# Kernel optimization log

Hardware: AMD Instinct MI355X
Metric: run time of the kernel (lower is better)

## Reference

```python
import jax, jax.numpy as jnp
import numpy as np

B, S, H, W, L = 16, 2048, 512, 4, 2  # batch, seq, projection_dim, width, n_layers
EPS = 1e-5


def _ln(x, g, b):
    m = jnp.mean(x, axis=-1, keepdims=True)
    v = jnp.mean((x - m) ** 2, axis=-1, keepdims=True)
    return g * (x - m) * jax.lax.rsqrt(v + EPS) + b


def setup_inputs() -> dict:
    key = jax.random.key(0)
    ks = jax.random.split(key, 24)
    s = 0.02
    d = {
        'inputs': jax.random.normal(ks[0], (B, S, H), jnp.float32),
        'left_padding': jax.random.normal(ks[1], (W, H), jnp.float32) * s,
        'right_padding': jax.random.normal(ks[2], (W, H), jnp.float32) * s,
        'Wl': jax.random.normal(ks[3], (W * H, H), jnp.float32) * s,
        'bl': jnp.zeros((H,), jnp.float32),
        'Wr': jax.random.normal(ks[4], (W * H, H), jnp.float32) * s,
        'br': jnp.zeros((H,), jnp.float32),
        'lw1': jax.random.normal(ks[5], (L, H, H), jnp.float32) * s,
        'lb1': jnp.zeros((L, H), jnp.float32),
        'lw2': jax.random.normal(ks[6], (L, H, H), jnp.float32) * s,
        'lb2': jnp.zeros((L, H), jnp.float32),
        'lg': jnp.ones((L, H), jnp.float32),
        'lbeta': jnp.zeros((L, H), jnp.float32),
        'rw1': jax.random.normal(ks[7], (L, H, H), jnp.float32) * s,
        'rb1': jnp.zeros((L, H), jnp.float32),
        'rw2': jax.random.normal(ks[8], (L, H, H), jnp.float32) * s,
        'rb2': jnp.zeros((L, H), jnp.float32),
        'rg': jnp.ones((L, H), jnp.float32),
        'rbeta': jnp.zeros((L, H), jnp.float32),
    }
    return d


def reference(inputs, left_padding, right_padding, Wl, bl, Wr, br,
              lw1, lb1, lw2, lb2, lg, lbeta,
              rw1, rb1, rw2, rb2, rg, rbeta):
    b, s, h = inputs.shape
    w = left_padding.shape[0]
    padded = jnp.concatenate([
        jnp.broadcast_to(left_padding, (b, w, h)), inputs,
        jnp.broadcast_to(right_padding, (b, w, h))], axis=1)  # [B, W+S+W, H]
    t = jnp.arange(s)[:, None]
    off = jnp.arange(w)[None, :]
    left = padded[:, t + off].reshape(b, s, w * h)           # rows [t, t+w)
    right = padded[:, t + (w + 1) + off].reshape(b, s, w * h)  # rows [t+w+1, t+2w+1)
    lo = jax.nn.relu(jnp.einsum('bsk,kh->bsh', left, Wl) + bl)
    ro = jax.nn.relu(jnp.einsum('bsk,kh->bsh', right, Wr) + br)
    layers = []
    for i in range(lw1.shape[0]):
        # SublayerConnection: x + FF(LayerNorm(x)); FF = w2(relu(w1(.)))
        lo = lo + jnp.einsum('bsh,hk->bsk', jax.nn.relu(
            jnp.einsum('bsh,hk->bsk', _ln(lo, lg[i], lbeta[i]), lw1[i]) + lb1[i]), lw2[i]) + lb2[i]
        ro = ro + jnp.einsum('bsh,hk->bsk', jax.nn.relu(
            jnp.einsum('bsh,hk->bsk', _ln(ro, rg[i], rbeta[i]), rw1[i]) + rb1[i]), rw2[i]) + rb2[i]
        layers.append(jnp.concatenate([lo, ro], axis=-1))  # [B,S,2H]
    stacked = jnp.stack(layers, axis=0)                 # [L,B,S,2H]
    all_layers = jnp.transpose(stacked, (0, 2, 1, 3))   # [L,S,B,2H]
    last_layers = layers[-1]                            # [B,S,2H]
    return all_layers, last_layers
```

## Files before the change

kernel.cpp:

```cpp
#include <hip/hip_runtime.h>
#include <stdint.h>

#define Bx   16
#define Sx   2048
#define Hx   512
#define Lx   2
#define PHx  2056
#define Mx   32768

typedef float f32x4  __attribute__((ext_vector_type(4)));
typedef __bf16 bf16x8 __attribute__((ext_vector_type(8)));
typedef unsigned short u16x8 __attribute__((ext_vector_type(8)));

typedef __attribute__((address_space(1))) void gvoid_t;
typedef __attribute__((address_space(3))) void lvoid_t;

__device__ __forceinline__ unsigned short f2bf(float f) {
  uint32_t u = __float_as_uint(f);
  u += 0x7FFFu + ((u >> 16) & 1u);
  return (unsigned short)(u >> 16);
}

__global__ __launch_bounds__(256) void build_padded_k(
    const float* __restrict__ inp, const float* __restrict__ lp,
    const float* __restrict__ rp, unsigned short* __restrict__ padded) {
  int64_t idx = (int64_t)blockIdx.x * 256 + threadIdx.x;
  int h = (int)(idx & 511);
  int64_t rowi = idx >> 9;
  int r = (int)(rowi % 2056);
  int b = (int)(rowi / 2056);
  float v;
  if (r < 4)          v = lp[r * 512 + h];
  else if (r < 2052)  v = inp[((int64_t)b * 2048 + (r - 4)) * 512 + h];
  else                v = rp[(r - 2052) * 512 + h];
  padded[idx] = f2bf(v);
}

__global__ __launch_bounds__(256) void prep_weights_k(
    const float* __restrict__ Wl, const float* __restrict__ Wr,
    const float* __restrict__ lw1, const float* __restrict__ lw2,
    const float* __restrict__ rw1, const float* __restrict__ rw2,
    unsigned short* __restrict__ Wlt, unsigned short* __restrict__ Wrt,
    unsigned short* __restrict__ lw1t, unsigned short* __restrict__ lw2t,
    unsigned short* __restrict__ rw1t, unsigned short* __restrict__ rw2t) {
  int idx = blockIdx.x * 256 + threadIdx.x;
  if (idx < 2097152) {
    int j = idx & 1048575;
    const float* src = (idx < 1048576) ? Wl : Wr;
    unsigned short* dst = (idx < 1048576) ? Wlt : Wrt;
    int n = j >> 11, k = j & 2047;
    dst[j] = f2bf(src[(int64_t)k * 512 + n]);
  } else {
    int j = idx - 2097152;
    int mat = j >> 18;
    int e = j & 262143;
    int arr = mat >> 1, layer = mat & 1;
    const float* srcs[4] = {lw1, lw2, rw1, rw2};
    unsigned short* dsts[4] = {lw1t, lw2t, rw1t, rw2t};
    const float* src = srcs[arr] + (int64_t)layer * 262144;
    unsigned short* dst = dsts[arr] + (int64_t)layer * 262144;
    int n = e >> 9, k = e & 511;
    dst[e] = f2bf(src[k * 512 + n]);
  }
}

__global__ __launch_bounds__(256) void ln_k(
    const float* __restrict__ x, int x_off,
    const float* __restrict__ g, const float* __restrict__ beta,
    unsigned short* __restrict__ xhat) {
  int row = blockIdx.x * 4 + (threadIdx.x >> 6);
  int lane = threadIdx.x & 63;
  const float4* xr = (const float4*)(x + (int64_t)row * 1024 + x_off);
  float4 u = xr[lane * 2], w = xr[lane * 2 + 1];
  float xs[8] = {u.x, u.y, u.z, u.w, w.x, w.y, w.z, w.w};
  float sum = 0.f, ss = 0.f;
#pragma unroll
  for (int t = 0; t < 8; t++) { sum += xs[t]; ss += xs[t] * xs[t]; }
#pragma unroll
  for (int o = 32; o > 0; o >>= 1) {
    sum += __shfl_xor(sum, o);
    ss  += __shfl_xor(ss, o);
  }
  float mean = sum * (1.0f / 512.0f);
  float var  = ss * (1.0f / 512.0f) - mean * mean;
  float rstd = rsqrtf(var + 1e-5f);
  const float4* g4 = (const float4*)g;
  const float4* b4 = (const float4*)beta;
  float4 ga = g4[lane * 2], gb = g4[lane * 2 + 1];
  float4 ba = b4[lane * 2], bb = b4[lane * 2 + 1];
  float gs[8] = {ga.x, ga.y, ga.z, ga.w, gb.x, gb.y, gb.z, gb.w};
  float bs[8] = {ba.x, ba.y, ba.z, ba.w, bb.x, bb.y, bb.z, bb.w};
  u16x8 val;
#pragma unroll
  for (int t = 0; t < 8; t++) val[t] = f2bf(gs[t] * (xs[t] - mean) * rstd + bs[t]);
  *(u16x8*)(xhat + (int64_t)row * 512 + lane * 8) = val;
}

template <int MODE>
__global__ __launch_bounds__(256) void gemm_k(
    const unsigned short* __restrict__ A, int64_t a_bstride, int a_off, int K,
    const unsigned short* __restrict__ Bt, const float* __restrict__ bias,
    float* __restrict__ C, unsigned short* __restrict__ Cb,
    int c_off, float* __restrict__ out0p) {
  __shared__ unsigned short sA[128 * 32];
  __shared__ unsigned short sB[128 * 32];
  const int tid  = threadIdx.x;
  const int lane = tid & 63;
  const int wave = tid >> 6;
  const int m0 = blockIdx.x * 128;
  const int n0 = blockIdx.y * 128;
  const int wm = (wave >> 1) * 64;
  const int wn = (wave & 1) * 64;
  const int fr = lane >> 4;
  const int fc = lane & 15;

  const unsigned short* Ablk =
      A + (int64_t)(m0 >> 11) * a_bstride + (int64_t)(m0 & 2047) * 512 + a_off;
  const unsigned short* Bblk = Bt + (int64_t)n0 * K;

  f32x4 acc[4][4] = {};

  const int t0 = tid, t1 = tid + 256;
  const int ar0 = t0 >> 2, ac0 = (t0 & 3) * 8;
  const int ar1 = t1 >> 2, ac1 = (t1 & 3) * 8;

  for (int k0 = 0; k0 < K; k0 += 32) {
    __builtin_amdgcn_global_load_lds(
        (gvoid_t*)(Ablk + (int64_t)ar0 * 512 + k0 + ac0),
        (lvoid_t*)(sA + t0 * 8), 16, 0, 0);
    __builtin_amdgcn_global_load_lds(
        (gvoid_t*)(Ablk + (int64_t)ar1 * 512 + k0 + ac1),
        (lvoid_t*)(sA + t1 * 8), 16, 0, 0);
    __builtin_amdgcn_global_load_lds(
        (gvoid_t*)(Bblk + (int64_t)ar0 * K + k0 + ac0),
        (lvoid_t*)(sB + t0 * 8), 16, 0, 0);
    __builtin_amdgcn_global_load_lds(
        (gvoid_t*)(Bblk + (int64_t)ar1 * K + k0 + ac1),
        (lvoid_t*)(sB + t1 * 8), 16, 0, 0);
    __syncthreads();

    bf16x8 af[4], bf[4];
#pragma unroll
    for (int i = 0; i < 4; i++)
      af[i] = *(const bf16x8*)(sA + (wm + i * 16 + fc) * 32 + fr * 8);
#pragma unroll
    for (int j = 0; j < 4; j++)
      bf[j] = *(const bf16x8*)(sB + (wn + j * 16 + fc) * 32 + fr * 8);
#pragma unroll
    for (int i = 0; i < 4; i++)
#pragma unroll
      for (int j = 0; j < 4; j++)
        acc[i][j] = __builtin_amdgcn_mfma_f32_16x16x32_bf16(af[i], bf[j], acc[i][j], 0, 0, 0);
    __syncthreads();
  }

  int col[4];
  float bv[4];
#pragma unroll
  for (int j = 0; j < 4; j++) {
    col[j] = n0 + wn + j * 16 + fc;
    bv[j] = bias[col[j]];
  }
  const int b_idx = m0 >> 11;
#pragma unroll
  for (int i = 0; i < 4; i++) {
#pragma unroll
    for (int r = 0; r < 4; r++) {
      const int m = m0 + wm + i * 16 + fr * 4 + r;
      if (MODE == 0) {
        const int64_t base = (int64_t)m * 1024 + c_off;
#pragma unroll
        for (int j = 0; j < 4; j++) {
          float v = acc[i][j][r] + bv[j];
          C[base + col[j]] = v > 0.f ? v : 0.f;
        }
      } else if (MODE == 1) {
        const int64_t base = (int64_t)m * 512;
#pragma unroll
        for (int j = 0; j < 4; j++) {
          float v = acc[i][j][r] + bv[j];
          Cb[base + col[j]] = f2bf(v > 0.f ? v : 0.f);
        }
      } else {
        const int64_t base = (int64_t)m * 1024 + c_off;
        const int s = m & 2047;
        const int64_t obase = (int64_t)s * 16384 + (int64_t)b_idx * 1024 + c_off;
#pragma unroll
        for (int j = 0; j < 4; j++) {
          float v = C[base + col[j]] + acc[i][j][r] + bv[j];
          C[base + col[j]] = v;
          out0p[obase + col[j]] = v;
        }
      }
    }
  }
}

extern "C" void kernel_launch(void* const* d_in, const int* in_sizes, int n_in,
                              void* d_out, int out_size, void* d_ws, size_t ws_size,
                              hipStream_t stream) {
  const float* inputs = (const float*)d_in[0];
  const float* lp     = (const float*)d_in[1];
  const float* rp     = (const float*)d_in[2];
  const float* Wl     = (const float*)d_in[3];
  const float* bl     = (const float*)d_in[4];
  const float* Wr     = (const float*)d_in[5];
  const float* br     = (const float*)d_in[6];
  const float* lw1    = (const float*)d_in[7];
  const float* lb1    = (const float*)d_in[8];
  const float* lw2    = (const float*)d_in[9];
  const float* lb2    = (const float*)d_in[10];
  const float* lg     = (const float*)d_in[11];
  const float* lbeta  = (const float*)d_in[12];
  const float* rw1    = (const float*)d_in[13];
  const float* rb1    = (const float*)d_in[14];
  const float* rw2    = (const float*)d_in[15];
  const float* rb2    = (const float*)d_in[16];
  const float* rg     = (const float*)d_in[17];
  const float* rbeta  = (const float*)d_in[18];

  float* out0 = (float*)d_out;
  float* out1 = out0 + (int64_t)Lx * Sx * Bx * 1024;

  char* w = (char*)d_ws;
  auto take = [&](size_t n) { char* p = w; w += (n + 255) & ~(size_t)255; return p; };
  unsigned short* padded = (unsigned short*)take((size_t)Bx * PHx * Hx * 2);
  unsigned short* Wlt    = (unsigned short*)take(2048ull * 512 * 2);
  unsigned short* Wrt    = (unsigned short*)take(2048ull * 512 * 2);
  unsigned short* lw1t   = (unsigned short*)take((size_t)Lx * 512 * 512 * 2);
  unsigned short* lw2t   = (unsigned short*)take((size_t)Lx * 512 * 512 * 2);
  unsigned short* rw1t   = (unsigned short*)take((size_t)Lx * 512 * 512 * 2);
  unsigned short* rw2t   = (unsigned short*)take((size_t)Lx * 512 * 512 * 2);
  unsigned short* xhat   = (unsigned short*)take((size_t)Mx * 512 * 2);
  unsigned short* hidden = (unsigned short*)take((size_t)Mx * 512 * 2);

  build_padded_k<<<65792, 256, 0, stream>>>(inputs, lp, rp, padded);
  prep_weights_k<<<16384, 256, 0, stream>>>(Wl, Wr, lw1, lw2, rw1, rw2,
                                            Wlt, Wrt, lw1t, lw2t, rw1t, rw2t);

  dim3 gg(256, 4);
  gemm_k<0><<<gg, 256, 0, stream>>>(padded, (int64_t)PHx * 512, 0, 2048, Wlt, bl,
                                    out1, nullptr, 0, nullptr);
  gemm_k<0><<<gg, 256, 0, stream>>>(padded, (int64_t)PHx * 512, 5 * 512, 2048, Wrt, br,
                                    out1, nullptr, 512, nullptr);

  for (int i = 0; i < Lx; i++) {
    for (int side = 0; side < 2; side++) {
      const float* g  = (side ? rg : lg) + i * 512;
      const float* be = (side ? rbeta : lbeta) + i * 512;
      const float* b1 = (side ? rb1 : lb1) + i * 512;
      const float* b2 = (side ? rb2 : lb2) + i * 512;
      const unsigned short* w1t = (side ? rw1t : lw1t) + (int64_t)i * 262144;
      const unsigned short* w2t = (side ? rw2t : lw2t) + (int64_t)i * 262144;

      ln_k<<<8192, 256, 0, stream>>>(out1, side * 512, g, be, xhat);
      gemm_k<1><<<gg, 256, 0, stream>>>(xhat, (int64_t)2048 * 512, 0, 512, w1t, b1,
                                        nullptr, hidden, 0, nullptr);
      gemm_k<2><<<gg, 256, 0, stream>>>(hidden, (int64_t)2048 * 512, 0, 512, w2t, b2,
                                        out1, nullptr, side * 512,
                                        out0 + (int64_t)i * Sx * Bx * 1024);
    }
  }
}
```

Before: 1.183 ms.

## Fuse LayerNorm into FFN GEMM via epilogue row stats, batch left/right sides

Removes the standalone LayerNorm kernel. The producing GEMM epilogues now write per-row partial sum and sum-of-squares, and the first FFN GEMM normalizes fp32 state rows while staging A into LDS. Left and right branches are batched into a single launch via blockIdx.z, which halves the launch count and doubles the grid. The padding build is vectorized and the weight transpose goes through LDS tiles. The cost is extra fp32 reads inside the GEMM A-load path (no async LDS load for A) and a one-pass variance formula.

```diff
diff --git a/kernel.cpp b/kernel.cpp
--- a/kernel.cpp
+++ b/kernel.cpp
@@ -24,16 +24,21 @@
 __global__ __launch_bounds__(256) void build_padded_k(
     const float* __restrict__ inp, const float* __restrict__ lp,
     const float* __restrict__ rp, unsigned short* __restrict__ padded) {
-  int64_t idx = (int64_t)blockIdx.x * 256 + threadIdx.x;
+  int64_t idx = ((int64_t)blockIdx.x * 256 + threadIdx.x) * 8;
   int h = (int)(idx & 511);
   int64_t rowi = idx >> 9;
   int r = (int)(rowi % 2056);
   int b = (int)(rowi / 2056);
-  float v;
-  if (r < 4)          v = lp[r * 512 + h];
-  else if (r < 2052)  v = inp[((int64_t)b * 2048 + (r - 4)) * 512 + h];
-  else                v = rp[(r - 2052) * 512 + h];
-  padded[idx] = f2bf(v);
+  const float* src;
+  if (r < 4)          src = lp + r * 512 + h;
+  else if (r < 2052)  src = inp + ((int64_t)b * 2048 + (r - 4)) * 512 + h;
+  else                src = rp + (r - 2052) * 512 + h;
+  float4 u = ((const float4*)src)[0];
+  float4 w = ((const float4*)src)[1];
+  u16x8 o;
+  o[0] = f2bf(u.x); o[1] = f2bf(u.y); o[2] = f2bf(u.z); o[3] = f2bf(u.w);
+  o[4] = f2bf(w.x); o[5] = f2bf(w.y); o[6] = f2bf(w.z); o[7] = f2bf(w.w);
+  *(u16x8*)(padded + idx) = o;
 }
 
 __global__ __launch_bounds__(256) void prep_weights_k(
@@ -43,65 +48,168 @@
     unsigned short* __restrict__ Wlt, unsigned short* __restrict__ Wrt,
     unsigned short* __restrict__ lw1t, unsigned short* __restrict__ lw2t,
     unsigned short* __restrict__ rw1t, unsigned short* __restrict__ rw2t) {
-  int idx = blockIdx.x * 256 + threadIdx.x;
-  if (idx < 2097152) {
-    int j = idx & 1048575;
-    const float* src = (idx < 1048576) ? Wl : Wr;
-    unsigned short* dst = (idx < 1048576) ? Wlt : Wrt;
-    int n = j >> 11, k = j & 2047;
-    dst[j] = f2bf(src[(int64_t)k * 512 + n]);
+  __shared__ unsigned short tl[32][36];
+  int b = blockIdx.x;
+  const float* src; unsigned short* dst; int K, tk, tn;
+  if (b < 2048) {
+    src = (b < 1024) ? Wl : Wr;
+    dst = (b < 1024) ? Wlt : Wrt;
+    int t = b & 1023; tk = t >> 4; tn = t & 15; K = 2048;
   } else {
-    int j = idx - 2097152;
-    int mat = j >> 18;
-    int e = j & 262143;
-    int arr = mat >> 1, layer = mat & 1;
-    const float* srcs[4] = {lw1, lw2, rw1, rw2};
-    unsigned short* dsts[4] = {lw1t, lw2t, rw1t, rw2t};
-    const float* src = srcs[arr] + (int64_t)layer * 262144;
-    unsigned short* dst = dsts[arr] + (int64_t)layer * 262144;
-    int n = e >> 9, k = e & 511;
-    dst[e] = f2bf(src[k * 512 + n]);
-  }
-}
-
-__global__ __launch_bounds__(256) void ln_k(
-    const float* __restrict__ x, int x_off,
-    const float* __restrict__ g, const float* __restrict__ beta,
-    unsigned short* __restrict__ xhat) {
-  int row = blockIdx.x * 4 + (threadIdx.x >> 6);
-  int lane = threadIdx.x & 63;
-  const float4* xr = (const float4*)(x + (int64_t)row * 1024 + x_off);
-  float4 u = xr[lane * 2], w = xr[lane * 2 + 1];
-  float xs[8] = {u.x, u.y, u.z, u.w, w.x, w.y, w.z, w.w};
-  float sum = 0.f, ss = 0.f;
-#pragma unroll
-  for (int t = 0; t < 8; t++) { sum += xs[t]; ss += xs[t] * xs[t]; }
-#pragma unroll
-  for (int o = 32; o > 0; o >>= 1) {
-    sum += __shfl_xor(sum, o);
-    ss  += __shfl_xor(ss, o);
-  }
-  float mean = sum * (1.0f / 512.0f);
-  float var  = ss * (1.0f / 512.0f) - mean * mean;
-  float rstd = rsqrtf(var + 1e-5f);
-  const float4* g4 = (const float4*)g;
-  const float4* b4 = (const float4*)beta;
-  float4 ga = g4[lane * 2], gb = g4[lane * 2 + 1];
-  float4 ba = b4[lane * 2], bb = b4[lane * 2 + 1];
-  float gs[8] = {ga.x, ga.y, ga.z, ga.w, gb.x, gb.y, gb.z, gb.w};
-  float bs[8] = {ba.x, ba.y, ba.z, ba.w, bb.x, bb.y, bb.z, bb.w};
-  u16x8 val;
-#pragma unroll
-  for (int t = 0; t < 8; t++) val[t] = f2bf(gs[t] * (xs[t] - mean) * rstd + bs[t]);
-  *(u16x8*)(xhat + (int64_t)row * 512 + lane * 8) = val;
-}
-
-template <int MODE>
+    int b2 = b - 2048;
+    int mat = b2 >> 8;
+    const float* srcs[8] = {lw1, lw1 + 262144, lw2, lw2 + 262144,
+                            rw1, rw1 + 262144, rw2, rw2 + 262144};
+    unsigned short* dsts[8] = {lw1t, lw1t + 262144, lw2t, lw2t + 262144,
+                               rw1t, rw1t + 262144, rw2t, rw2t + 262144};
+    src = srcs[mat]; dst = dsts[mat];
+    int tt = b2 & 255; tk = tt >> 4; tn = tt & 15; K = 512;
+  }
+  int t = threadIdx.x;
+  int rr = t >> 3, c4 = (t & 7) * 4;
+  float4 v = *(const float4*)(src + (int64_t)(tk * 32 + rr) * 512 + tn * 32 + c4);
+  tl[c4 + 0][rr] = f2bf(v.x);
+  tl[c4 + 1][rr] = f2bf(v.y);
+  tl[c4 + 2][rr] = f2bf(v.z);
+  tl[c4 + 3][rr] = f2bf(v.w);
+  __syncthreads();
+  int nn = t >> 3, k4 = (t & 7) * 4;
+  ushort4 o = {tl[nn][k4], tl[nn][k4 + 1], tl[nn][k4 + 2], tl[nn][k4 + 3]};
+  *(ushort4*)(dst + (int64_t)(tn * 32 + nn) * K + tk * 32 + k4) = o;
+}
+
+template <int MODE, bool STATS>
 __global__ __launch_bounds__(256) void gemm_k(
-    const unsigned short* __restrict__ A, int64_t a_bstride, int a_off, int K,
-    const unsigned short* __restrict__ Bt, const float* __restrict__ bias,
-    float* __restrict__ C, unsigned short* __restrict__ Cb,
-    int c_off, float* __restrict__ out0p) {
+    const unsigned short* __restrict__ A0, const unsigned short* __restrict__ A1,
+    int64_t a_bstride, int a_off_per_z, int K,
+    const unsigned short* __restrict__ Bt0, const unsigned short* __restrict__ Bt1,
+    const float* __restrict__ bias0, const float* __restrict__ bias1,
+    float* __restrict__ C, float* __restrict__ out0p, float* __restrict__ P) {
+  __shared__ unsigned short sA[128 * 32];
+  __shared__ unsigned short sB[128 * 32];
+  __shared__ float sls[128][2][2];
+  const int tid  = threadIdx.x;
+  const int lane = tid & 63;
+  const int wave = tid >> 6;
+  const int m0 = blockIdx.x * 128;
+  const int n0 = blockIdx.y * 128;
+  const int z  = blockIdx.z;
+  const int wm = (wave >> 1) * 64;
+  const int wn = (wave & 1) * 64;
+  const int fr = lane >> 4;
+  const int fc = lane & 15;
+
+  const unsigned short* A  = z ? A1 : A0;
+  const unsigned short* Bt = z ? Bt1 : Bt0;
+  const float* bias = z ? bias1 : bias0;
+  const int a_off = z * a_off_per_z;
+  const int c_off = z * 512;
+
+  const unsigned short* Ablk =
+      A + (int64_t)(m0 >> 11) * a_bstride + (int64_t)(m0 & 2047) * 512 + a_off;
+  const unsigned short* Bblk = Bt + (int64_t)n0 * K;
+
+  f32x4 acc[4][4] = {};
+
+  const int t0 = tid, t1 = tid + 256;
+  const int ar0 = t0 >> 2, ac0 = (t0 & 3) * 8;
+  const int ar1 = t1 >> 2, ac1 = (t1 & 3) * 8;
+
+  for (int k0 = 0; k0 < K; k0 += 32) {
+    __builtin_amdgcn_global_load_lds(
+        (gvoid_t*)(Ablk + (int64_t)ar0 * 512 + k0 + ac0),
+        (lvoid_t*)(sA + t0 * 8), 16, 0, 0);
+    __builtin_amdgcn_global_load_lds(
+        (gvoid_t*)(Ablk + (int64_t)ar1 * 512 + k0 + ac1),
+        (lvoid_t*)(sA + t1 * 8), 16, 0, 0);
+    __builtin_amdgcn_global_load_lds(
+        (gvoid_t*)(Bblk + (int64_t)ar0 * K + k0 + ac0),
+        (lvoid_t*)(sB + t0 * 8), 16, 0, 0);
+    __builtin_amdgcn_global_load_lds(
+        (gvoid_t*)(Bblk + (int64_t)ar1 * K + k0 + ac1),
+        (lvoid_t*)(sB + t1 * 8), 16, 0, 0);
+    __syncthreads();
+
+    bf16x8 af[4], bf[4];
+#pragma unroll
+    for (int i = 0; i < 4; i++)
+      af[i] = *(const bf16x8*)(sA + (wm + i * 16 + fc) * 32 + fr * 8);
+#pragma unroll
+    for (int j = 0; j < 4; j++)
+      bf[j] = *(const bf16x8*)(sB + (wn + j * 16 + fc) * 32 + fr * 8);
+#pragma unroll
+    for (int i = 0; i < 4; i++)
+#pragma unroll
+      for (int j = 0; j < 4; j++)
+        acc[i][j] = __builtin_amdgcn_mfma_f32_16x16x32_bf16(af[i], bf[j], acc[i][j], 0, 0, 0);
+    __syncthreads();
+  }
+
+  int col[4];
+  float bv[4];
+#pragma unroll
+  for (int j = 0; j < 4; j++) {
+    col[j] = n0 + wn + j * 16 + fc;
+    bv[j] = bias[col[j]];
+  }
+  const int b_idx = m0 >> 11;
+#pragma unroll
+  for (int i = 0; i < 4; i++) {
+#pragma unroll
+    for (int r = 0; r < 4; r++) {
+      const int m = m0 + wm + i * 16 + fr * 4 + r;
+      const int64_t base = (int64_t)m * 1024 + c_off;
+      float vs[4];
+      if (MODE == 0) {
+#pragma unroll
+        for (int j = 0; j < 4; j++) {
+          float v = acc[i][j][r] + bv[j];
+          v = v > 0.f ? v : 0.f;
+          C[base + col[j]] = v;
+          vs[j] = v;
+        }
+      } else {
+        const int s = m & 2047;
+        const int64_t obase = (int64_t)s * 16384 + (int64_t)b_idx * 1024 + c_off;
+#pragma unroll
+        for (int j = 0; j < 4; j++) {
+          float v = C[base + col[j]] + acc[i][j][r] + bv[j];
+          C[base + col[j]] = v;
+          out0p[obase + col[j]] = v;
+          vs[j] = v;
+        }
+      }
+      if (STATS) {
+        float s1 = vs[0] + vs[1] + vs[2] + vs[3];
+        float s2 = vs[0] * vs[0] + vs[1] * vs[1] + vs[2] * vs[2] + vs[3] * vs[3];
+#pragma unroll
+        for (int o = 1; o < 16; o <<= 1) {
+          s1 += __shfl_xor(s1, o);
+          s2 += __shfl_xor(s2, o);
+        }
+        if (fc == 0) {
+          int li = (wave >> 1) * 64 + i * 16 + fr * 4 + r;
+          sls[li][wave & 1][0] = s1;
+          sls[li][wave & 1][1] = s2;
+        }
+      }
+    }
+  }
+  if (STATS) {
+    __syncthreads();
+    int li = tid >> 1, comp = tid & 1;
+    float v = sls[li][0][comp] + sls[li][1][comp];
+    P[(((int64_t)z * 4 + blockIdx.y) * Mx + m0 + li) * 2 + comp] = v;
+  }
+}
+
+__global__ __launch_bounds__(256) void gemm_ln_k(
+    const float* __restrict__ state, const float* __restrict__ P,
+    const float* __restrict__ g0, const float* __restrict__ g1p,
+    const float* __restrict__ be0, const float* __restrict__ be1,
+    const unsigned short* __restrict__ Bt0, const unsigned short* __restrict__ Bt1,
+    const float* __restrict__ bias0, const float* __restrict__ bias1,
+    unsigned short* __restrict__ hidden) {
   __shared__ unsigned short sA[128 * 32];
   __shared__ unsigned short sB[128 * 32];
   const int tid  = threadIdx.x;
@@ -109,34 +217,72 @@
   const int wave = tid >> 6;
   const int m0 = blockIdx.x * 128;
   const int n0 = blockIdx.y * 128;
+  const int z  = blockIdx.z;
   const int wm = (wave >> 1) * 64;
   const int wn = (wave & 1) * 64;
   const int fr = lane >> 4;
   const int fc = lane & 15;
 
-  const unsigned short* Ablk =
-      A + (int64_t)(m0 >> 11) * a_bstride + (int64_t)(m0 & 2047) * 512 + a_off;
-  const unsigned short* Bblk = Bt + (int64_t)n0 * K;
+  const unsigned short* Bt = z ? Bt1 : Bt0;
+  const float* bias = z ? bias1 : bias0;
+  const float* g    = z ? g1p : g0;
+  const float* be   = z ? be1 : be0;
+  const int c_off = z * 512;
+  const unsigned short* Bblk = Bt + (int64_t)n0 * 512;
+
+  const int row  = tid >> 1;
+  const int half = tid & 1;
+  const int m = m0 + row;
+  const float* srcrow = state + (int64_t)m * 1024 + c_off + half * 16;
+
+  float s1 = 0.f, s2 = 0.f;
+#pragma unroll
+  for (int nb = 0; nb < 4; nb++) {
+    s1 += P[(((int64_t)z * 4 + nb) * Mx + m) * 2 + 0];
+    s2 += P[(((int64_t)z * 4 + nb) * Mx + m) * 2 + 1];
+  }
+  const float mean = s1 * (1.0f / 512.0f);
+  const float rstd = rsqrtf(s2 * (1.0f / 512.0f) - mean * mean + 1e-5f);
 
   f32x4 acc[4][4] = {};
 
   const int t0 = tid, t1 = tid + 256;
-  const int ar0 = t0 >> 2, ac0 = (t0 & 3) * 8;
-  const int ar1 = t1 >> 2, ac1 = (t1 & 3) * 8;
-
-  for (int k0 = 0; k0 < K; k0 += 32) {
-    __builtin_amdgcn_global_load_lds(
-        (gvoid_t*)(Ablk + (int64_t)ar0 * 512 + k0 + ac0),
-        (lvoid_t*)(sA + t0 * 8), 16, 0, 0);
-    __builtin_amdgcn_global_load_lds(
-        (gvoid_t*)(Ablk + (int64_t)ar1 * 512 + k0 + ac1),
-        (lvoid_t*)(sA + t1 * 8), 16, 0, 0);
-    __builtin_amdgcn_global_load_lds(
-        (gvoid_t*)(Bblk + (int64_t)ar0 * K + k0 + ac0),
+  const int br0 = t0 >> 2, bc0 = (t0 & 3) * 8;
+  const int br1 = t1 >> 2, bc1 = (t1 & 3) * 8;
+
+  for (int k0 = 0; k0 < 512; k0 += 32) {
+    __builtin_amdgcn_global_load_lds(
+        (gvoid_t*)(Bblk + (int64_t)br0 * 512 + k0 + bc0),
         (lvoid_t*)(sB + t0 * 8), 16, 0, 0);
     __builtin_amdgcn_global_load_lds(
-        (gvoid_t*)(Bblk + (int64_t)ar1 * K + k0 + ac1),
+        (gvoid_t*)(Bblk + (int64_t)br1 * 512 + k0 + bc1),
         (lvoid_t*)(sB + t1 * 8), 16, 0, 0);
+
+    const float* sp = srcrow + k0;
+    float xs[16], gs[16], bs[16];
+    *(float4*)(xs + 0)  = ((const float4*)sp)[0];
+    *(float4*)(xs + 4)  = ((const float4*)sp)[1];
+    *(float4*)(xs + 8)  = ((const float4*)sp)[2];
+    *(float4*)(xs + 12) = ((const float4*)sp)[3];
+    const float* gp = g + k0 + half * 16;
+    const float* bp = be + k0 + half * 16;
+    *(float4*)(gs + 0)  = ((const float4*)gp)[0];
+    *(float4*)(gs + 4)  = ((const float4*)gp)[1];
+    *(float4*)(gs + 8)  = ((const float4*)gp)[2];
+    *(float4*)(gs + 12) = ((const float4*)gp)[3];
+    *(float4*)(bs + 0)  = ((const float4*)bp)[0];
+    *(float4*)(bs + 4)  = ((const float4*)bp)[1];
+    *(float4*)(bs + 8)  = ((const float4*)bp)[2];
+    *(float4*)(bs + 12) = ((const float4*)bp)[3];
+    u16x8 o0, o1;
+#pragma unroll
+    for (int t = 0; t < 8; t++)
+      o0[t] = f2bf((xs[t] - mean) * rstd * gs[t] + bs[t]);
+#pragma unroll
+    for (int t = 0; t < 8; t++)
+      o1[t] = f2bf((xs[t + 8] - mean) * rstd * gs[t + 8] + bs[t + 8]);
+    *(u16x8*)(sA + row * 32 + half * 16)     = o0;
+    *(u16x8*)(sA + row * 32 + half * 16 + 8) = o1;
     __syncthreads();
 
     bf16x8 af[4], bf[4];
@@ -154,6 +300,7 @@
     __syncthreads();
   }
 
+  unsigned short* Cb = hidden + (int64_t)z * Mx * 512;
   int col[4];
   float bv[4];
 #pragma unroll
@@ -161,36 +308,16 @@
     col[j] = n0 + wn + j * 16 + fc;
     bv[j] = bias[col[j]];
   }
-  const int b_idx = m0 >> 11;
 #pragma unroll
   for (int i = 0; i < 4; i++) {
 #pragma unroll
     for (int r = 0; r < 4; r++) {
-      const int m = m0 + wm + i * 16 + fr * 4 + r;
-      if (MODE == 0) {
-        const int64_t base = (int64_t)m * 1024 + c_off;
-#pragma unroll
-        for (int j = 0; j < 4; j++) {
-          float v = acc[i][j][r] + bv[j];
-          C[base + col[j]] = v > 0.f ? v : 0.f;
-        }
-      } else if (MODE == 1) {
-        const int64_t base = (int64_t)m * 512;
-#pragma unroll
-        for (int j = 0; j < 4; j++) {
-          float v = acc[i][j][r] + bv[j];
-          Cb[base + col[j]] = f2bf(v > 0.f ? v : 0.f);
-        }
-      } else {
-        const int64_t base = (int64_t)m * 1024 + c_off;
-        const int s = m & 2047;
-        const int64_t obase = (int64_t)s * 16384 + (int64_t)b_idx * 1024 + c_off;
-#pragma unroll
-        for (int j = 0; j < 4; j++) {
-          float v = C[base + col[j]] + acc[i][j][r] + bv[j];
-          C[base + col[j]] = v;
-          out0p[obase + col[j]] = v;
-        }
+      const int mm = m0 + wm + i * 16 + fr * 4 + r;
+      const int64_t base = (int64_t)mm * 512;
+#pragma unroll
+      for (int j = 0; j < 4; j++) {
+        float v = acc[i][j][r] + bv[j];
+        Cb[base + col[j]] = f2bf(v > 0.f ? v : 0.f);
       }
     }
   }
@@ -231,34 +358,33 @@
   unsigned short* lw2t   = (unsigned short*)take((size_t)Lx * 512 * 512 * 2);
   unsigned short* rw1t   = (unsigned short*)take((size_t)Lx * 512 * 512 * 2);
   unsigned short* rw2t   = (unsigned short*)take((size_t)Lx * 512 * 512 * 2);
-  unsigned short* xhat   = (unsigned short*)take((size_t)Mx * 512 * 2);
-  unsigned short* hidden = (unsigned short*)take((size_t)Mx * 512 * 2);
-
-  build_padded_k<<<65792, 256, 0, stream>>>(inputs, lp, rp, padded);
-  prep_weights_k<<<16384, 256, 0, stream>>>(Wl, Wr, lw1, lw2, rw1, rw2,
-                                            Wlt, Wrt, lw1t, lw2t, rw1t, rw2t);
-
-  dim3 gg(256, 4);
-  gemm_k<0><<<gg, 256, 0, stream>>>(padded, (int64_t)PHx * 512, 0, 2048, Wlt, bl,
-                                    out1, nullptr, 0, nullptr);
-  gemm_k<0><<<gg, 256, 0, stream>>>(padded, (int64_t)PHx * 512, 5 * 512, 2048, Wrt, br,
-                                    out1, nullptr, 512, nullptr);
+  unsigned short* hidden = (unsigned short*)take((size_t)2 * Mx * 512 * 2);
+  float*          Pst    = (float*)take((size_t)2 * 4 * Mx * 2 * 4);
+
+  build_padded_k<<<8224, 256, 0, stream>>>(inputs, lp, rp, padded);
+  prep_weights_k<<<4096, 256, 0, stream>>>(Wl, Wr, lw1, lw2, rw1, rw2,
+                                           Wlt, Wrt, lw1t, lw2t, rw1t, rw2t);
+
+  dim3 gg(256, 4, 2);
+  gemm_k<0, true><<<gg, 256, 0, stream>>>(
+      padded, padded, (int64_t)PHx * 512, 5 * 512, 2048,
+      Wlt, Wrt, bl, br, out1, nullptr, Pst);
 
   for (int i = 0; i < Lx; i++) {
-    for (int side = 0; side < 2; side++) {
-      const float* g  = (side ? rg : lg) + i * 512;
-      const float* be = (side ? rbeta : lbeta) + i * 512;
-      const float* b1 = (side ? rb1 : lb1) + i * 512;
-      const float* b2 = (side ? rb2 : lb2) + i * 512;
-      const unsigned short* w1t = (side ? rw1t : lw1t) + (int64_t)i * 262144;
-      const unsigned short* w2t = (side ? rw2t : lw2t) + (int64_t)i * 262144;
-
-      ln_k<<<8192, 256, 0, stream>>>(out1, side * 512, g, be, xhat);
-      gemm_k<1><<<gg, 256, 0, stream>>>(xhat, (int64_t)2048 * 512, 0, 512, w1t, b1,
-                                        nullptr, hidden, 0, nullptr);
-      gemm_k<2><<<gg, 256, 0, stream>>>(hidden, (int64_t)2048 * 512, 0, 512, w2t, b2,
-                                        out1, nullptr, side * 512,
-                                        out0 + (int64_t)i * Sx * Bx * 1024);
+    gemm_ln_k<<<gg, 256, 0, stream>>>(
+        out1, Pst, lg + i * 512, rg + i * 512, lbeta + i * 512, rbeta + i * 512,
+        lw1t + (int64_t)i * 262144, rw1t + (int64_t)i * 262144,
+        lb1 + i * 512, rb1 + i * 512, hidden);
+    if (i == 0) {
+      gemm_k<2, true><<<gg, 256, 0, stream>>>(
+          hidden, hidden + (int64_t)Mx * 512, (int64_t)2048 * 512, 0, 512,
+          lw2t, rw2t, lb2, rb2, out1, out0, Pst);
+    } else {
+      gemm_k<2, false><<<gg, 256, 0, stream>>>(
+          hidden, hidden + (int64_t)Mx * 512, (int64_t)2048 * 512, 0, 512,
+          lw2t + (int64_t)i * 262144, rw2t + (int64_t)i * 262144,
+          lb2 + i * 512, rb2 + i * 512, out1,
+          out0 + (int64_t)i * Sx * Bx * 1024, nullptr);
     }
   }
 }
```

Result: faster. 1.075 ms (-9.1%).
